# Kernel optimization log

Measured on AMD Instinct MI355X. Metric: run time of the kernel, lower is better.

Reference implementation:

```python
import jax, jax.numpy as jnp
import numpy as np

B, P, N, DIM = 2, 2, 1024, 256
HEADS, DH = 8, 64
INNER = HEADS * DH
HW = 32
C = HW * HW  # conv channels = h1*h2 = 1024
LN_EPS = 1e-5
BN_EPS = 1e-5


def setup_inputs() -> dict:
    key = jax.random.key(0)
    ks = jax.random.split(key, 10)
    return {
        "x": jax.random.normal(ks[0], (B, P, N, DIM), jnp.float32),
        "ln_g": jnp.ones((DIM,), jnp.float32),
        "ln_b": jnp.zeros((DIM,), jnp.float32),
        "w_qkv": jax.random.normal(ks[1], (DIM, 3 * INNER), jnp.float32) * DIM ** -0.5,
        "w_conv1": jax.random.normal(ks[2], (C, 2), jnp.float32) * 0.7,
        "w_conv2": jax.random.normal(ks[3], (C, 2), jnp.float32) * 0.7,
        "w_1x1": jax.random.normal(ks[4], (C, C), jnp.float32) * C ** -0.5,
        "bn_g": jnp.ones((C,), jnp.float32),
        "bn_b": jnp.zeros((C,), jnp.float32),
        "bn_m": jax.random.normal(ks[5], (C,), jnp.float32) * 0.1,
        "bn_v": jax.random.uniform(ks[6], (C,), jnp.float32, minval=0.5, maxval=1.5),
        "w_out": jax.random.normal(ks[7], (INNER, DIM), jnp.float32) * INNER ** -0.5,
        "b_out": jnp.zeros((DIM,), jnp.float32),
    }


def _dw_conv_w(a, w):
    # depthwise (1,2) kernel, reflection pad right by 1 (pad value = col W-2)
    ap = jnp.concatenate([a, a[..., -2:-1]], axis=-1)
    return ap[..., :-1] * w[:, 0][None, :, None, None] + ap[..., 1:] * w[:, 1][None, :, None, None]


def _dw_conv_h(a, w):
    # depthwise (2,1) kernel, reflection pad bottom by 1 (pad value = row H-2)
    ap = jnp.concatenate([a, a[:, :, -2:-1, :]], axis=2)
    return ap[:, :, :-1, :] * w[:, 0][None, :, None, None] + ap[:, :, 1:, :] * w[:, 1][None, :, None, None]


def reference(x, ln_g, ln_b, w_qkv, w_conv1, w_conv2, w_1x1, bn_g, bn_b, bn_m, bn_v, w_out, b_out):
    b, p, n, dim = x.shape
    # LayerNorm
    mu = jnp.mean(x, axis=-1, keepdims=True)
    var = jnp.mean(jnp.square(x - mu), axis=-1, keepdims=True)
    xn = (x - mu) * jax.lax.rsqrt(var + LN_EPS) * ln_g + ln_b
    # QKV projection, split heads
    qkv = xn @ w_qkv  # (b,p,n,3*inner)
    q, k, v = jnp.split(qkv, 3, axis=-1)
    split_heads = lambda t: t.reshape(b, p, n, HEADS, DH).transpose(0, 1, 3, 2, 4)
    q, k, v = map(split_heads, (q, k, v))  # (b,p,h,n,d)
    dots = jnp.einsum('bphnd,bphmd->bphnm', q, k) * (DH ** -0.5)  # (b,p,h,n,n)
    # rearrange scores: n=(h1 w1), m=(h2 w2) -> channels (h1 h2), spatial (w1 w2)
    a = dots.reshape(b, p, HEADS, HW, HW, HW, HW)
    a = a.transpose(0, 1, 2, 3, 5, 4, 6).reshape(b * p * HEADS, C, HW, HW)
    a = _dw_conv_w(a, w_conv1)
    a = _dw_conv_h(a, w_conv2)
    # 1x1 conv (no bias) + BatchNorm (inference) + SiLU
    a = jnp.einsum('bchw,oc->bohw', a, w_1x1)
    inv = jax.lax.rsqrt(bn_v + BN_EPS)
    a = (a - bn_m[None, :, None, None]) * (inv * bn_g)[None, :, None, None] + bn_b[None, :, None, None]
    a = a * jax.nn.sigmoid(a)
    # rearrange back to (b,p,h,n,n)
    a = a.reshape(b, p, HEADS, HW, HW, HW, HW).transpose(0, 1, 2, 3, 5, 4, 6).reshape(b, p, HEADS, n, n)
    attn = jax.nn.softmax(a, axis=-1)
    out = jnp.einsum('bphnm,bphmd->bphnd', attn, v)
    out = out.transpose(0, 1, 3, 2, 4).reshape(b, p, n, INNER)
    return out @ w_out + b_out
```

## Files before the change

kernel.cpp:

```cpp
#include <hip/hip_runtime.h>
#include <hip/hip_fp16.h>


#define DEV __device__ __forceinline__

typedef __attribute__((ext_vector_type(8))) _Float16 f16x8;
typedef __attribute__((ext_vector_type(4))) float f32x4;
typedef __attribute__((ext_vector_type(8))) unsigned short u16x8;

DEV float h2f_bits(unsigned short u) { __half h; *reinterpret_cast<unsigned short*>(&h) = u; return __half2float(h); }
DEV unsigned short f2h_bits(float f) { __half h = __float2half(f); return *reinterpret_cast<unsigned short*>(&h); }

__global__ __launch_bounds__(256) void prep_kernel(
    const float* __restrict__ wqkv, const float* __restrict__ w1x1,
    const float* __restrict__ wout,
    __half* __restrict__ WQKVT, __half* __restrict__ W1X1H, __half* __restrict__ WOTT) {
  int i0 = blockIdx.x * 256 + threadIdx.x;
  int stride = gridDim.x * 256;
  for (int i = i0; i < 1536 * 256; i += stride) {
    int j = i >> 8, k = i & 255;
    WQKVT[i] = __float2half(wqkv[k * 1536 + j]);
  }
  for (int i = i0; i < 1024 * 1024; i += stride) {
    int o = i >> 10, p = i & 1023;
    int blk = p >> 5, r = p & 31, a = r >> 3, bb = r & 7;
    int h1 = (blk >> 2) * 4 + a, h2 = (blk & 3) * 8 + bb;
    W1X1H[i] = __float2half(w1x1[o * 1024 + h1 * 32 + h2]);
  }
  for (int i = i0; i < 256 * 512; i += stride) {
    int j = i >> 9, k = i & 511;
    WOTT[i] = __float2half(wout[k * 256 + j]);
  }
}

__global__ __launch_bounds__(256) void ln_kernel(const float* __restrict__ x,
    const float* __restrict__ g, const float* __restrict__ b, __half* __restrict__ XN) {
  int row = blockIdx.x;
  int tid = threadIdx.x, lane = tid & 63, wid = tid >> 6;
  float xv = x[(size_t)row * 256 + tid];
  float s = xv, q = xv * xv;
#pragma unroll
  for (int off = 32; off; off >>= 1) { s += __shfl_xor(s, off); q += __shfl_xor(q, off); }
  __shared__ float rs[4], rq[4];
  if (lane == 0) { rs[wid] = s; rq[wid] = q; }
  __syncthreads();
  s = rs[0] + rs[1] + rs[2] + rs[3];
  q = rq[0] + rq[1] + rq[2] + rq[3];
  float mu = s * (1.f / 256.f);
  float var = q * (1.f / 256.f) - mu * mu;
  float r = rsqrtf(var + 1e-5f);
  XN[(size_t)row * 256 + tid] = __float2half((xv - mu) * r * g[tid] + b[tid]);
}

template <int BM, int BN, int BK, int WGN, int FM, int FN, class Epi>
__global__ __launch_bounds__(256) void gemm_bt(
    const __half* __restrict__ A, long long aStride,
    const __half* __restrict__ B, long long bStride,
    int K, Epi epi) {
  constexpr int CPR = BK / 8;
  constexpr int NCA = (BM * BK) / (8 * 256);
  constexpr int NCB = (BN * BK) / (8 * 256);
  constexpr int KSUB = BK / 32;
  __shared__ __align__(16) __half smA[2][BM * BK];
  __shared__ __align__(16) __half smB[2][BN * BK];
  const int tid = threadIdx.x;
  const int lane = tid & 63, wid = tid >> 6;
  const int wr = wid / WGN, wc = wid % WGN;
  const int gx = gridDim.x, gxy = gridDim.x * gridDim.y;
  const int nwg = gxy * gridDim.z;
  const int b_lin = blockIdx.x + blockIdx.y * gx + blockIdx.z * gxy;
  const int logical = (b_lin & 7) * (nwg >> 3) + (b_lin >> 3);
  const int bx = logical % gx, by = (logical / gx) % gridDim.y, bz = logical / gxy;
  const int img = bz;
  const int row0 = bx * BM;
  const int col0 = by * BN;
  const __half* Ab = A + (size_t)((long long)img * aStride);
  const __half* Bb = B + (size_t)((long long)img * bStride);
  f32x4 acc[FM][FN] = {};
  const int lr = lane & 15;
  const int kq = lane >> 4;

  auto swz = [](int c, int r) -> int {
    return (CPR == 8) ? (c ^ (r & 7)) : (c ^ ((r >> 1) & 3));
  };

  const __half* pA[NCA]; int dA[NCA];
  const __half* pB[NCB]; int dB[NCB];
#pragma unroll
  for (int it = 0; it < NCA; ++it) {
    int e = it * 256 + tid, r = e / CPR, c = e % CPR;
    pA[it] = Ab + (size_t)(row0 + r) * K + swz(c, r) * 8;
    dA[it] = r * BK + c * 8;
  }
#pragma unroll
  for (int it = 0; it < NCB; ++it) {
    int e = it * 256 + tid, r = e / CPR, c = e % CPR;
    pB[it] = Bb + (size_t)(col0 + r) * K + swz(c, r) * 8;
    dB[it] = r * BK + c * 8;
  }

  auto stage = [&](int buf, int kt) {
#pragma unroll
    for (int it = 0; it < NCA; ++it)
      __builtin_amdgcn_global_load_lds(
          (const __attribute__((address_space(1))) unsigned int*)(pA[it] + kt),
          (__attribute__((address_space(3))) unsigned int*)(&smA[buf][dA[it]]),
          16, 0, 0);
#pragma unroll
    for (int it = 0; it < NCB; ++it)
      __builtin_amdgcn_global_load_lds(
          (const __attribute__((address_space(1))) unsigned int*)(pB[it] + kt),
          (__attribute__((address_space(3))) unsigned int*)(&smB[buf][dB[it]]),
          16, 0, 0);
  };

  const int NT = K / BK;
  stage(0, 0);
  __syncthreads();
  int cur = 0;
  for (int t = 0; t < NT; ++t) {
    if (t + 1 < NT) stage(cur ^ 1, (t + 1) * BK);
#pragma unroll
    for (int kk = 0; kk < KSUB; ++kk) {
      f16x8 av[FM], bv[FN];
#pragma unroll
      for (int i = 0; i < FM; ++i) {
        int row = wr * FM * 16 + i * 16 + lr;
        int ch = swz(kk * 4 + kq, lr);
        av[i] = *reinterpret_cast<const f16x8*>(&smA[cur][row * BK + ch * 8]);
      }
#pragma unroll
      for (int j = 0; j < FN; ++j) {
        int row = wc * FN * 16 + j * 16 + lr;
        int ch = swz(kk * 4 + kq, lr);
        bv[j] = *reinterpret_cast<const f16x8*>(&smB[cur][row * BK + ch * 8]);
      }
#pragma unroll
      for (int i = 0; i < FM; ++i)
#pragma unroll
        for (int j = 0; j < FN; ++j)
          acc[i][j] = __builtin_amdgcn_mfma_f32_16x16x32_f16(av[i], bv[j], acc[i][j], 0, 0, 0);
    }
    __syncthreads();
    cur ^= 1;
  }

  const int orow = row0 + wr * FM * 16 + (lane >> 4) * 4;
  const int ocol = col0 + wc * FN * 16 + lr;
#pragma unroll
  for (int i = 0; i < FM; ++i)
#pragma unroll
    for (int j = 0; j < FN; ++j)
#pragma unroll
      for (int q = 0; q < 4; ++q)
        epi.store(img, orow + i * 16 + q, ocol + j * 16, acc[i][j][q]);
}

struct EpiQKV {
  __half *Q, *K, *V;
  DEV void store(int, int t, int j, float v) const {
    int part = j >> 9, inner = j & 511;
    int h = inner >> 6, d = inner & 63;
    int bp = t >> 10, n = t & 1023;
    size_t img = (size_t)(bp * 8 + h);
    if (part == 0)       Q[(img * 1024 + n) * 64 + d] = __float2half(v * 0.125f);
    else if (part == 1)  K[(img * 1024 + n) * 64 + d] = __float2half(v);
    else                 V[(img * 64 + d) * 1024 + n] = __float2half(v);
  }
};
struct EpiPV {
  __half* O;
  DEV void store(int img, int n, int d, float v) const {
    int bp = img >> 3, h = img & 7;
    O[((size_t)(bp * 1024 + n)) * 512 + h * 64 + d] = __float2half(v);
  }
};
struct EpiOut {
  float* out; const float* bias;
  DEV void store(int, int t, int j, float v) const {
    out[(size_t)t * 256 + j] = v + bias[j];
  }
};

__global__ __launch_bounds__(512) void qkconv_kernel(
    const __half* __restrict__ Q, const __half* __restrict__ Km,
    const float* __restrict__ wc1, const float* __restrict__ wc2,
    __half* __restrict__ AC) {
  constexpr int NP = 132;
  __shared__ __align__(16) char LDS[77824];
  __half* smA = (__half*)LDS;
  __half* smB = (__half*)(LDS + 16384);
  __half* Dt  = (__half*)LDS;
  __half* T   = (__half*)(LDS + 67584);
  const int tid = threadIdx.x;
  const int lane = tid & 63, wid = tid >> 6;
  const int wr = wid >> 2, wc = wid & 3;
  const int gx = gridDim.x, gxy = gx * gridDim.y;
  const int nwg = gxy * gridDim.z;
  const int b_lin = blockIdx.x + blockIdx.y * gx + blockIdx.z * gxy;
  const int logical = (b_lin & 7) * (nwg >> 3) + (b_lin >> 3);
  const int bx = logical % gx, by = (logical / gx) % gridDim.y, bz = logical / gxy;
  const int img = bz, row0 = bx * 128, col0 = by * 256;
  const __half* Qi = Q + ((size_t)img << 16);
  const __half* Ki = Km + ((size_t)img << 16);

#pragma unroll
  for (int it = 0; it < 2; ++it) {
    int e = it * 512 + tid, r = e >> 3, c = e & 7, sc = c ^ (r & 7);
    __builtin_amdgcn_global_load_lds(
        (const __attribute__((address_space(1))) unsigned int*)(Qi + (size_t)(row0 + r) * 64 + sc * 8),
        (__attribute__((address_space(3))) unsigned int*)(smA + r * 64 + c * 8), 16, 0, 0);
  }
#pragma unroll
  for (int it = 0; it < 4; ++it) {
    int e = it * 512 + tid, r = e >> 3, c = e & 7, sc = c ^ (r & 7);
    __builtin_amdgcn_global_load_lds(
        (const __attribute__((address_space(1))) unsigned int*)(Ki + (size_t)(col0 + r) * 64 + sc * 8),
        (__attribute__((address_space(3))) unsigned int*)(smB + r * 64 + c * 8), 16, 0, 0);
  }
  __syncthreads();

  const int lr = lane & 15, kq = lane >> 4;
  f32x4 acc[4][4] = {};
#pragma unroll
  for (int kk = 0; kk < 2; ++kk) {
    const int ch = (kk * 4 + kq) ^ (lr & 7);
    f16x8 av[4], bv[4];
#pragma unroll
    for (int i = 0; i < 4; ++i)
      av[i] = *reinterpret_cast<const f16x8*>(&smA[(wr * 64 + i * 16 + lr) * 64 + ch * 8]);
#pragma unroll
    for (int j = 0; j < 4; ++j)
      bv[j] = *reinterpret_cast<const f16x8*>(&smB[(wc * 64 + j * 16 + lr) * 64 + ch * 8]);
#pragma unroll
    for (int i = 0; i < 4; ++i)
#pragma unroll
      for (int j = 0; j < 4; ++j)
        acc[i][j] = __builtin_amdgcn_mfma_f32_16x16x32_f16(av[i], bv[j], acc[i][j], 0, 0, 0);
  }
  __syncthreads();

#pragma unroll
  for (int i = 0; i < 4; ++i) {
    int n0 = wr * 64 + i * 16 + kq * 4;
#pragma unroll
    for (int j = 0; j < 4; ++j) {
      int m = wc * 64 + j * 16 + lr;
      ushort4 o4;
      o4.x = f2h_bits(acc[i][j][0]); o4.y = f2h_bits(acc[i][j][1]);
      o4.z = f2h_bits(acc[i][j][2]); o4.w = f2h_bits(acc[i][j][3]);
      *reinterpret_cast<ushort4*>(Dt + m * NP + n0) = o4;
    }
  }
  __syncthreads();

  const int w2i = tid >> 7;
  const int b_  = (tid >> 4) & 7;
  const int a_  = (tid >> 2) & 3;
  const int w1q = (tid & 3) * 8;
  const int cch = (bx * 4 + a_) * 32 + (by * 8 + b_);
  const float u0 = wc1[2 * cch], u1 = wc1[2 * cch + 1];
  const float v0 = wc2[2 * cch], v1 = wc2[2 * cch + 1];
  const int cblk = (bx * 4 + by) * 32;
  __half* ACi = AC + ((size_t)img << 20);
  const int w1o = (tid >> 2) & 31, ck = tid & 3;

  for (int pass = 0; pass < 8; ++pass) {
    const int w2 = pass * 4 + w2i;
    const int w2n = (w2 < 31) ? w2 + 1 : 30;
    const __half* r0 = Dt + (b_ * 32 + w2) * NP + a_ * 32 + w1q;
    const __half* r1 = Dt + (b_ * 32 + w2n) * NP + a_ * 32 + w1q;
    float X[9];
    {
      ushort4 x0a = *reinterpret_cast<const ushort4*>(r0);
      ushort4 x0b = *reinterpret_cast<const ushort4*>(r0 + 4);
      ushort4 x1a = *reinterpret_cast<const ushort4*>(r1);
      ushort4 x1b = *reinterpret_cast<const ushort4*>(r1 + 4);
      X[0] = u0 * h2f_bits(x0a.x) + u1 * h2f_bits(x1a.x);
      X[1] = u0 * h2f_bits(x0a.y) + u1 * h2f_bits(x1a.y);
      X[2] = u0 * h2f_bits(x0a.z) + u1 * h2f_bits(x1a.z);
      X[3] = u0 * h2f_bits(x0a.w) + u1 * h2f_bits(x1a.w);
      X[4] = u0 * h2f_bits(x0b.x) + u1 * h2f_bits(x1b.x);
      X[5] = u0 * h2f_bits(x0b.y) + u1 * h2f_bits(x1b.y);
      X[6] = u0 * h2f_bits(x0b.z) + u1 * h2f_bits(x1b.z);
      X[7] = u0 * h2f_bits(x0b.w) + u1 * h2f_bits(x1b.w);
      X[8] = u0 * __half2float(r0[8]) + u1 * __half2float(r1[8]);
    }
#pragma unroll
    for (int k = 0; k < 8; ++k) {
      float ov = (w1q + k < 31) ? (v0 * X[k] + v1 * X[k + 1])
                                : (v0 * X[7] + v1 * X[6]);
      T[(w2i * 32 + w1q + k) * 40 + a_ * 8 + b_] = __float2half(ov);
    }
    __syncthreads();
    {
      const int w2o = pass * 4 + (tid >> 7);
      u16x8 v = *reinterpret_cast<const u16x8*>(T + ((tid >> 7) * 32 + w1o) * 40 + ck * 8);
      *reinterpret_cast<u16x8*>(ACi + (size_t)(w1o * 32 + w2o) * 1024 + cblk + ck * 8) = v;
    }
    __syncthreads();
  }
}

struct Epi1x1F {
  __half* P;
  const float *g, *b, *m, *vv;
  DEV void finalize(int img, int ob, int cb, int lane, f32x4 (&acc)[4][4]) const {
    const int lr = lane & 15, kq = lane >> 4;
    __half* Pi = P + ((size_t)img << 20);
#pragma unroll
    for (int ih = 0; ih < 2; ++ih) {
#pragma unroll
      for (int sh = 0; sh < 2; ++sh) {
        float v[2][2][4];
        float mx = -1e30f;
#pragma unroll
        for (int di = 0; di < 2; ++di) {
          int i = ih * 2 + di;
#pragma unroll
          for (int q = 0; q < 4; ++q) {
            int o = ob + i * 16 + kq * 4 + q;
            float sc = rsqrtf(vv[o] + 1e-5f) * g[o];
            float mo = m[o], bo = b[o];
#pragma unroll
            for (int dj = 0; dj < 2; ++dj) {
              float t = (acc[i][sh * 2 + dj][q] - mo) * sc + bo;
              t = t / (1.f + __expf(-t));
              v[di][dj][q] = t;
              mx = fmaxf(mx, t);
            }
          }
        }
#pragma unroll
        for (int off = 32; off; off >>= 1) mx = fmaxf(mx, __shfl_xor(mx, off));
        float sm = 0.f;
#pragma unroll
        for (int di = 0; di < 2; ++di)
#pragma unroll
          for (int dj = 0; dj < 2; ++dj)
#pragma unroll
            for (int q = 0; q < 4; ++q) {
              float e = __expf(v[di][dj][q] - mx);
              v[di][dj][q] = e; sm += e;
            }
#pragma unroll
        for (int off = 32; off; off >>= 1) sm += __shfl_xor(sm, off);
        float inv = 1.f / sm;
#pragma unroll
        for (int di = 0; di < 2; ++di) {
          int i = ih * 2 + di;
#pragma unroll
          for (int q = 0; q < 4; ++q) {
            int o = ob + i * 16 + kq * 4 + q;
            size_t nhi = (size_t)(o >> 5) * 32;
            int mlo = (o & 31) * 32;
#pragma unroll
            for (int dj = 0; dj < 2; ++dj) {
              int s = cb + (sh * 2 + dj) * 16 + lr;
              Pi[(nhi + (s >> 5)) * 1024 + mlo + (s & 31)] = __float2half(v[di][dj][q] * inv);
            }
          }
        }
      }
    }
  }
};

template <class Epi>
__global__ __launch_bounds__(512, 4) void gemm1x1(
    const __half* __restrict__ A,
    const __half* __restrict__ B, long long bStride,
    int K, Epi epi) {
  __shared__ __align__(16) __half smA[2][256 * 32];
  __shared__ __align__(16) __half smB[2][128 * 32];
  const int tid = threadIdx.x;
  const int lane = tid & 63, wid = tid >> 6;
  const int wr = wid >> 1, wc = wid & 1;
  const int gx = gridDim.x, gxy = gx * gridDim.y;
  const int nwg = gxy * gridDim.z;
  const int b_lin = blockIdx.x + blockIdx.y * gx + blockIdx.z * gxy;
  const int logical = (b_lin & 7) * (nwg >> 3) + (b_lin >> 3);
  const int bx = logical % gx, by = (logical / gx) % gridDim.y, bz = logical / gxy;
  const int img = bz, row0 = bx * 256, col0 = by * 128;
  const __half* Ab = A;
  const __half* Bb = B + (size_t)((long long)img * bStride);

  const __half* pA[2]; int dA[2];
#pragma unroll
  for (int it = 0; it < 2; ++it) {
    int e = it * 512 + tid, r = e >> 2, c = e & 3, sc = c ^ ((r >> 1) & 3);
    pA[it] = Ab + (size_t)(row0 + r) * K + sc * 8;
    dA[it] = r * 32 + c * 8;
  }
  const __half* pB1; int dB1;
  {
    int r = tid >> 2, c = tid & 3, sc = c ^ ((r >> 1) & 3);
    pB1 = Bb + (size_t)(col0 + r) * K + sc * 8;
    dB1 = r * 32 + c * 8;
  }
  auto stage = [&](int buf, int kt) {
#pragma unroll
    for (int it = 0; it < 2; ++it)
      __builtin_amdgcn_global_load_lds(
          (const __attribute__((address_space(1))) unsigned int*)(pA[it] + kt),
          (__attribute__((address_space(3))) unsigned int*)(&smA[buf][dA[it]]),
          16, 0, 0);
    __builtin_amdgcn_global_load_lds(
        (const __attribute__((address_space(1))) unsigned int*)(pB1 + kt),
        (__attribute__((address_space(3))) unsigned int*)(&smB[buf][dB1]),
        16, 0, 0);
  };

  const int lr = lane & 15, kq = lane >> 4;
  const int ch = kq ^ ((lr >> 1) & 3);
  const int aOff = (wr * 64 + lr) * 32 + ch * 8;
  const int bOff = (wc * 64 + lr) * 32 + ch * 8;
  f32x4 acc[4][4] = {};

  const int NT = K / 32;
  stage(0, 0);
  __syncthreads();
  int cur = 0;
  for (int t = 0; t < NT; ++t) {
    if (t + 1 < NT) stage(cur ^ 1, (t + 1) * 32);
    f16x8 av[4], bv[4];
#pragma unroll
    for (int i = 0; i < 4; ++i)
      av[i] = *reinterpret_cast<const f16x8*>(&smA[cur][aOff + i * 512]);
#pragma unroll
    for (int j = 0; j < 4; ++j)
      bv[j] = *reinterpret_cast<const f16x8*>(&smB[cur][bOff + j * 512]);
    __builtin_amdgcn_s_setprio(1);
#pragma unroll
    for (int i = 0; i < 4; ++i)
#pragma unroll
      for (int j = 0; j < 4; ++j)
        acc[i][j] = __builtin_amdgcn_mfma_f32_16x16x32_f16(av[i], bv[j], acc[i][j], 0, 0, 0);
    __builtin_amdgcn_s_setprio(0);
    __syncthreads();
    cur ^= 1;
  }
  epi.finalize(img, row0 + wr * 64, col0 + wc * 64, lane, acc);
}

extern "C" void kernel_launch(void* const* d_in, const int* in_sizes, int n_in,
                              void* d_out, int out_size, void* d_ws, size_t ws_size,
                              hipStream_t stream) {
  const float* x     = (const float*)d_in[0];
  const float* ln_g  = (const float*)d_in[1];
  const float* ln_b  = (const float*)d_in[2];
  const float* w_qkv = (const float*)d_in[3];
  const float* wc1   = (const float*)d_in[4];
  const float* wc2   = (const float*)d_in[5];
  const float* w1x1  = (const float*)d_in[6];
  const float* bn_g  = (const float*)d_in[7];
  const float* bn_b  = (const float*)d_in[8];
  const float* bn_m  = (const float*)d_in[9];
  const float* bn_v  = (const float*)d_in[10];
  const float* w_out = (const float*)d_in[11];
  const float* b_out = (const float*)d_in[12];
  float* out = (float*)d_out;

  const size_t MB = 1024 * 1024;
  char* ws = (char*)d_ws;
  __half* Pb = (__half*)ws;
  __half* ACb = (__half*)(ws + 64 * MB);
  char* p = ws + 128 * MB;
  __half* XN    = (__half*)p; p += 2 * MB;
  __half* WQKVT = (__half*)p; p += 1536 * 256 * 2;
  __half* W1X1H = (__half*)p; p += 2 * MB;
  __half* WOTT  = (__half*)p; p += 256 * 512 * 2;
  __half* Qb    = (__half*)p; p += 4 * MB;
  __half* Kb    = (__half*)p; p += 4 * MB;
  __half* Vtb   = (__half*)p; p += 4 * MB;
  __half* Ob    = (__half*)p; p += 4 * MB;

  prep_kernel<<<2048, 256, 0, stream>>>(w_qkv, w1x1, w_out, WQKVT, W1X1H, WOTT);
  ln_kernel<<<4096, 256, 0, stream>>>(x, ln_g, ln_b, XN);

  { EpiQKV e{Qb, Kb, Vtb};
    gemm_bt<128, 128, 64, 2, 4, 4, EpiQKV><<<dim3(32, 12, 1), 256, 0, stream>>>(
        XN, 0, WQKVT, 0, 256, e); }

  qkconv_kernel<<<dim3(8, 4, 32), 512, 0, stream>>>(Qb, Kb, wc1, wc2, ACb);

  { Epi1x1F e{Pb, bn_g, bn_b, bn_m, bn_v};
    gemm1x1<Epi1x1F><<<dim3(4, 8, 32), 512, 0, stream>>>(
        W1X1H, ACb, 1 << 20, 1024, e); }

  { EpiPV e{Ob};
    gemm_bt<128, 64, 64, 2, 4, 2, EpiPV><<<dim3(8, 1, 32), 256, 0, stream>>>(
        Pb, 1 << 20, Vtb, 65536, 1024, e); }

  { EpiOut e{out, b_out};
    gemm_bt<64, 64, 64, 2, 2, 2, EpiOut><<<dim3(64, 4, 1), 256, 0, stream>>>(
        Ob, 0, WOTT, 0, 512, e); }
}
```

Baseline: 188.7 us.

## Fuse softmax-probability times V GEMM into the 1x1 conv GEMM epilogue

The 1x1-conv GEMM tile (256 channels x 128 spatial) already covers complete softmax rows. It now writes the normalized probabilities into a swizzled LDS buffer that reuses the GEMM staging memory, then multiplies them by V with MFMA inside the same kernel. This drops the separate PV GEMM launch and the 64MB fp16 round trip of the probability tensor through global memory. The cost is extra work and LDS use in the epilogue, with V read directly from global memory by each block.

```diff
diff --git a/kernel.cpp b/kernel.cpp
--- a/kernel.cpp
+++ b/kernel.cpp
@@ -168,13 +168,6 @@
     else                 V[(img * 64 + d) * 1024 + n] = __float2half(v);
   }
 };
-struct EpiPV {
-  __half* O;
-  DEV void store(int img, int n, int d, float v) const {
-    int bp = img >> 3, h = img & 7;
-    O[((size_t)(bp * 1024 + n)) * 512 + h * 64 + d] = __float2half(v);
-  }
-};
 struct EpiOut {
   float* out; const float* bias;
   DEV void store(int, int t, int j, float v) const {
@@ -302,77 +295,18 @@
   }
 }
 
-struct Epi1x1F {
-  __half* P;
-  const float *g, *b, *m, *vv;
-  DEV void finalize(int img, int ob, int cb, int lane, f32x4 (&acc)[4][4]) const {
-    const int lr = lane & 15, kq = lane >> 4;
-    __half* Pi = P + ((size_t)img << 20);
-#pragma unroll
-    for (int ih = 0; ih < 2; ++ih) {
-#pragma unroll
-      for (int sh = 0; sh < 2; ++sh) {
-        float v[2][2][4];
-        float mx = -1e30f;
-#pragma unroll
-        for (int di = 0; di < 2; ++di) {
-          int i = ih * 2 + di;
-#pragma unroll
-          for (int q = 0; q < 4; ++q) {
-            int o = ob + i * 16 + kq * 4 + q;
-            float sc = rsqrtf(vv[o] + 1e-5f) * g[o];
-            float mo = m[o], bo = b[o];
-#pragma unroll
-            for (int dj = 0; dj < 2; ++dj) {
-              float t = (acc[i][sh * 2 + dj][q] - mo) * sc + bo;
-              t = t / (1.f + __expf(-t));
-              v[di][dj][q] = t;
-              mx = fmaxf(mx, t);
-            }
-          }
-        }
-#pragma unroll
-        for (int off = 32; off; off >>= 1) mx = fmaxf(mx, __shfl_xor(mx, off));
-        float sm = 0.f;
-#pragma unroll
-        for (int di = 0; di < 2; ++di)
-#pragma unroll
-          for (int dj = 0; dj < 2; ++dj)
-#pragma unroll
-            for (int q = 0; q < 4; ++q) {
-              float e = __expf(v[di][dj][q] - mx);
-              v[di][dj][q] = e; sm += e;
-            }
-#pragma unroll
-        for (int off = 32; off; off >>= 1) sm += __shfl_xor(sm, off);
-        float inv = 1.f / sm;
-#pragma unroll
-        for (int di = 0; di < 2; ++di) {
-          int i = ih * 2 + di;
-#pragma unroll
-          for (int q = 0; q < 4; ++q) {
-            int o = ob + i * 16 + kq * 4 + q;
-            size_t nhi = (size_t)(o >> 5) * 32;
-            int mlo = (o & 31) * 32;
-#pragma unroll
-            for (int dj = 0; dj < 2; ++dj) {
-              int s = cb + (sh * 2 + dj) * 16 + lr;
-              Pi[(nhi + (s >> 5)) * 1024 + mlo + (s & 31)] = __float2half(v[di][dj][q] * inv);
-            }
-          }
-        }
-      }
-    }
-  }
-};
-
-template <class Epi>
-__global__ __launch_bounds__(512, 4) void gemm1x1(
+__global__ __launch_bounds__(512, 4) void gemm1x1pv(
     const __half* __restrict__ A,
     const __half* __restrict__ B, long long bStride,
-    int K, Epi epi) {
-  __shared__ __align__(16) __half smA[2][256 * 32];
-  __shared__ __align__(16) __half smB[2][128 * 32];
+    const __half* __restrict__ Vt,
+    int K,
+    const float* __restrict__ g, const float* __restrict__ b,
+    const float* __restrict__ m, const float* __restrict__ vv,
+    __half* __restrict__ O) {
+  __shared__ __align__(16) char LDSRAW[65536];
+  __half* smA = (__half*)LDSRAW;
+  __half* smB = (__half*)(LDSRAW + 32768);
+  __half* Plds = (__half*)LDSRAW;
   const int tid = threadIdx.x;
   const int lane = tid & 63, wid = tid >> 6;
   const int wr = wid >> 1, wc = wid & 1;
@@ -403,11 +337,11 @@
     for (int it = 0; it < 2; ++it)
       __builtin_amdgcn_global_load_lds(
           (const __attribute__((address_space(1))) unsigned int*)(pA[it] + kt),
-          (__attribute__((address_space(3))) unsigned int*)(&smA[buf][dA[it]]),
+          (__attribute__((address_space(3))) unsigned int*)(&smA[buf * 8192 + dA[it]]),
           16, 0, 0);
     __builtin_amdgcn_global_load_lds(
         (const __attribute__((address_space(1))) unsigned int*)(pB1 + kt),
-        (__attribute__((address_space(3))) unsigned int*)(&smB[buf][dB1]),
+        (__attribute__((address_space(3))) unsigned int*)(&smB[buf * 4096 + dB1]),
         16, 0, 0);
   };
 
@@ -426,10 +360,10 @@
     f16x8 av[4], bv[4];
 #pragma unroll
     for (int i = 0; i < 4; ++i)
-      av[i] = *reinterpret_cast<const f16x8*>(&smA[cur][aOff + i * 512]);
+      av[i] = *reinterpret_cast<const f16x8*>(&smA[cur * 8192 + aOff + i * 512]);
 #pragma unroll
     for (int j = 0; j < 4; ++j)
-      bv[j] = *reinterpret_cast<const f16x8*>(&smB[cur][bOff + j * 512]);
+      bv[j] = *reinterpret_cast<const f16x8*>(&smB[cur * 4096 + bOff + j * 512]);
     __builtin_amdgcn_s_setprio(1);
 #pragma unroll
     for (int i = 0; i < 4; ++i)
@@ -440,7 +374,84 @@
     __syncthreads();
     cur ^= 1;
   }
-  epi.finalize(img, row0 + wr * 64, col0 + wc * 64, lane, acc);
+  const int ob = row0 + wr * 64;
+#pragma unroll
+  for (int ih = 0; ih < 2; ++ih) {
+#pragma unroll
+    for (int sh = 0; sh < 2; ++sh) {
+      float v[2][2][4];
+      float mx = -1e30f;
+#pragma unroll
+      for (int di = 0; di < 2; ++di) {
+        int i = ih * 2 + di;
+#pragma unroll
+        for (int q = 0; q < 4; ++q) {
+          int o = ob + i * 16 + kq * 4 + q;
+          float sc = rsqrtf(vv[o] + 1e-5f) * g[o];
+          float mo = m[o], bo = b[o];
+#pragma unroll
+          for (int dj = 0; dj < 2; ++dj) {
+            float t = (acc[i][sh * 2 + dj][q] - mo) * sc + bo;
+            t = t / (1.f + __expf(-t));
+            v[di][dj][q] = t;
+            mx = fmaxf(mx, t);
+          }
+        }
+      }
+#pragma unroll
+      for (int off = 32; off; off >>= 1) mx = fmaxf(mx, __shfl_xor(mx, off));
+      float sm = 0.f;
+#pragma unroll
+      for (int di = 0; di < 2; ++di)
+#pragma unroll
+        for (int dj = 0; dj < 2; ++dj)
+#pragma unroll
+          for (int q = 0; q < 4; ++q) {
+            float e = __expf(v[di][dj][q] - mx);
+            v[di][dj][q] = e; sm += e;
+          }
+#pragma unroll
+      for (int off = 32; off; off >>= 1) sm += __shfl_xor(sm, off);
+      float inv = 1.f / sm;
+      const int ri = (wr * 2 + ih) * 4 + wc * 2 + sh;
+      const int sw = (ri & 7) << 3;
+      __half* Prow = Plds + ri * 1024;
+#pragma unroll
+      for (int di = 0; di < 2; ++di)
+#pragma unroll
+        for (int q = 0; q < 4; ++q) {
+          int mo_ = (di * 16 + kq * 4 + q) * 32;
+#pragma unroll
+          for (int dj = 0; dj < 2; ++dj) {
+            int mm = mo_ + dj * 16 + lr;
+            Prow[mm ^ sw] = __float2half(v[di][dj][q] * inv);
+          }
+        }
+    }
+  }
+  __syncthreads();
+  {
+    const int rt = wid >> 2, dt = wid & 3;
+    const int arow = rt * 16 + lr;
+    const int asw = (arow & 7) << 3;
+    const __half* Vw = Vt + ((size_t)img << 16) + (size_t)(dt * 16 + lr) * 1024;
+    const __half* Pr = Plds + arow * 1024;
+    f32x4 acc2 = {};
+#pragma unroll 8
+    for (int kk = 0; kk < 32; ++kk) {
+      int m0 = kk * 32 + kq * 8;
+      f16x8 a = *reinterpret_cast<const f16x8*>(&Pr[m0 ^ asw]);
+      f16x8 bb = *reinterpret_cast<const f16x8*>(&Vw[m0]);
+      acc2 = __builtin_amdgcn_mfma_f32_16x16x32_f16(a, bb, acc2, 0, 0, 0);
+    }
+#pragma unroll
+    for (int q = 0; q < 4; ++q) {
+      int ri = rt * 16 + kq * 4 + q;
+      int n = (bx * 8 + (ri >> 2)) * 32 + by * 4 + (ri & 3);
+      int d = dt * 16 + lr;
+      O[((size_t)((img >> 3) * 1024 + n)) * 512 + (img & 7) * 64 + d] = __float2half(acc2[q]);
+    }
+  }
 }
 
 extern "C" void kernel_launch(void* const* d_in, const int* in_sizes, int n_in,
@@ -463,7 +474,6 @@
 
   const size_t MB = 1024 * 1024;
   char* ws = (char*)d_ws;
-  __half* Pb = (__half*)ws;
   __half* ACb = (__half*)(ws + 64 * MB);
   char* p = ws + 128 * MB;
   __half* XN    = (__half*)p; p += 2 * MB;
@@ -484,13 +494,8 @@
 
   qkconv_kernel<<<dim3(8, 4, 32), 512, 0, stream>>>(Qb, Kb, wc1, wc2, ACb);
 
-  { Epi1x1F e{Pb, bn_g, bn_b, bn_m, bn_v};
-    gemm1x1<Epi1x1F><<<dim3(4, 8, 32), 512, 0, stream>>>(
-        W1X1H, ACb, 1 << 20, 1024, e); }
-
-  { EpiPV e{Ob};
-    gemm_bt<128, 64, 64, 2, 4, 2, EpiPV><<<dim3(8, 1, 32), 256, 0, stream>>>(
-        Pb, 1 << 20, Vtb, 65536, 1024, e); }
+  gemm1x1pv<<<dim3(4, 8, 32), 512, 0, stream>>>(
+      W1X1H, ACb, 1 << 20, Vtb, 1024, bn_g, bn_b, bn_m, bn_v, Ob);
 
   { EpiOut e{out, b_out};
     gemm_bt<64, 64, 64, 2, 2, 2, EpiOut><<<dim3(64, 4, 1), 256, 0, stream>>>(
```

Result: slower. 193.9 us (+2.8%).
